# Performance work log

Hardware: AMD Instinct MI355X
Metric: run time of the kernel (lower is better)

## Reference

```python
import jax, jax.numpy as jnp
import numpy as np

IMAGE_W = 640
IMAGE_H = 640
TOP_N = 1000
MIN_SCORE = 0.05
NMS_THR = 0.5
MAX_DET = 100
NUM_CLASSES = 80
STRIDES = [8, 16, 32, 64, 128]
BASE_SIZES = [32, 64, 128, 256, 512]
NEG = jnp.float32(-1e9)


def _make_anchors(batch):
    # standard RetinaNet grid anchors: 3 ratios x 3 scales per location
    per_level = []
    ratios = np.array([0.5, 1.0, 2.0])
    scales = np.array([2.0 ** 0, 2.0 ** (1.0 / 3.0), 2.0 ** (2.0 / 3.0)])
    for stride, base in zip(STRIDES, BASE_SIZES):
        g = IMAGE_W // stride
        ws, hs = [], []
        for r in ratios:
            for s in scales:
                a = base * s
                ws.append(a * np.sqrt(1.0 / r))
                hs.append(a * np.sqrt(r))
        ws = np.array(ws)[None, :]
        hs = np.array(hs)[None, :]
        c = (np.arange(g) + 0.5) * stride
        cxg, cyg = np.meshgrid(c, c)
        cxg = cxg.reshape(-1, 1)
        cyg = cyg.reshape(-1, 1)
        anch = np.stack([cxg - 0.5 * ws, cyg - 0.5 * hs, cxg + 0.5 * ws, cyg + 0.5 * hs], axis=-1)
        anch = anch.reshape(-1, 4).astype(np.float32)  # [g*g*9, 4]
        anch = np.broadcast_to(anch[None], (batch,) + anch.shape).copy()
        per_level.append(jnp.asarray(anch))
    return per_level


def setup_inputs() -> dict:
    key = jax.random.key(0)
    ks = jax.random.split(key, 10)
    B = 8
    ns = [(IMAGE_W // s) ** 2 * 9 for s in STRIDES]
    anchors = _make_anchors(B)
    inp = {}
    for i, n in enumerate(ns):
        inp[f"cls{i}"] = jax.random.uniform(ks[i], (B, n, NUM_CLASSES), dtype=jnp.float32)
        inp[f"reg{i}"] = jax.random.normal(ks[5 + i], (B, n, 4), dtype=jnp.float32) * 0.5
        inp[f"anc{i}"] = anchors[i]
    return inp


def _filter_level(cls_h, reg_h, anc):
    scores = jnp.max(cls_h, axis=2)           # [B, N]
    classes = jnp.argmax(cls_h, axis=2)       # [B, N] int
    if scores.shape[1] >= TOP_N:
        scores, idx = jax.lax.top_k(scores, TOP_N)
        classes = jnp.take_along_axis(classes, idx, axis=1)
        reg_h = jnp.take_along_axis(reg_h, idx[:, :, None], axis=1)
        anc = jnp.take_along_axis(anc, idx[:, :, None], axis=1)
    return scores, classes, reg_h, anc


def _decode(reg, anc):
    # snap tx,ty,tw,th to x1,y1,x2,y2 with int truncation + clamping (as original)
    wh = anc[..., 2:] - anc[..., :2]
    ctr = anc[..., :2] + 0.5 * wh
    r = reg * jnp.array([0.1, 0.1, 0.2, 0.2], reg.dtype)
    pwh = jnp.exp(r[..., 2:]) * wh
    pctr = r[..., :2] * wh + ctr
    b = jnp.concatenate([pctr - 0.5 * pwh, pctr + 0.5 * pwh], axis=-1)
    b = b.astype(jnp.int32)  # truncation toward zero, matches torch .int()
    b = jnp.stack([
        jnp.maximum(b[..., 0], 0),
        jnp.maximum(b[..., 1], 0),
        jnp.minimum(b[..., 2], IMAGE_W - 1),
        jnp.minimum(b[..., 3], IMAGE_H - 1),
    ], axis=-1)
    return b.astype(jnp.float32)


def _nms_one(scores, classes, boxes):
    # greedy NMS on fixed-size arrays with masking (equivalent to sort+while loop)
    valid = scores > MIN_SCORE
    areas = (boxes[:, 2] - boxes[:, 0]) * (boxes[:, 3] - boxes[:, 1])
    live = jnp.where(valid, scores, NEG)

    def step(live, _):
        idx = jnp.argmax(live)
        has = live[idx] > NEG * 0.5
        tb = boxes[idx]
        o_s = jnp.where(has, scores[idx], jnp.float32(-1.0))
        o_c = jnp.where(has, classes[idx].astype(jnp.float32), jnp.float32(-1.0))
        o_b = jnp.where(has, tb, -jnp.ones((4,), jnp.float32))
        tl = jnp.maximum(boxes[:, :2], tb[:2])
        br = jnp.minimum(boxes[:, 2:], tb[2:])
        owh = jnp.clip(br - tl, 0.0)
        inter = owh[:, 0] * owh[:, 1]
        union = jnp.clip(areas[idx] + areas - inter, 1e-4)
        iou = inter / union
        live = live.at[idx].set(NEG)  # remove the selected box itself
        live = jnp.where(has & (iou >= NMS_THR), NEG, live)
        return live, (o_s, o_c, o_b)

    _, (out_s, out_c, out_b) = jax.lax.scan(step, live, None, length=MAX_DET)
    return out_s, out_c, out_b


def reference(cls0, cls1, cls2, cls3, cls4, reg0, reg1, reg2, reg3, reg4,
              anc0, anc1, anc2, anc3, anc4):
    cls_heads = [cls0, cls1, cls2, cls3, cls4]
    reg_heads = [reg0, reg1, reg2, reg3, reg4]
    anchors = [anc0, anc1, anc2, anc3, anc4]
    fs, fc, fr, fa = [], [], [], []
    for c, r, a in zip(cls_heads, reg_heads, anchors):
        s, cl, r, a = _filter_level(c, r, a)
        fs.append(s); fc.append(cl); fr.append(r); fa.append(a)
    scores = jnp.concatenate(fs, axis=1)      # [B, 4125]
    classes = jnp.concatenate(fc, axis=1)
    regs = jnp.concatenate(fr, axis=1)
    ancs = jnp.concatenate(fa, axis=1)
    boxes = _decode(regs, ancs)               # [B, 4125, 4]
    batch_scores, batch_classes, batch_bboxes = jax.vmap(_nms_one)(scores, classes, boxes)
    return batch_scores, batch_classes, batch_bboxes
```

## Files before the change

kernel.cpp:

```cpp
#include <hip/hip_runtime.h>
#include <cmath>

#define NB      8
#define NANCH   76725
#define SSTRIDE 76800
#define CAPP    4352
#define NCAND   4125
#define TIECAP  256
#define MAXDET  100
#define BPI2    1201
#define ZWORDS  148992

struct Ptrs {
    const float* cls[5];
    const float* reg[5];
    const float* anc[5];
};

__device__ __forceinline__ void level_of(int i, int& lvl, int& n, int& N) {
    if (i < 57600)      { lvl = 0; n = i;         N = 57600; }
    else if (i < 72000) { lvl = 1; n = i - 57600; N = 14400; }
    else if (i < 75600) { lvl = 2; n = i - 72000; N = 3600;  }
    else if (i < 76500) { lvl = 3; n = i - 75600; N = 900;   }
    else                { lvl = 4; n = i - 76500; N = 225;   }
}

__device__ __forceinline__ void decode_box(const Ptrs& p, int b, int i, float out[4]) {
    int lvl, n, N; level_of(i, lvl, n, N);
    const float* r = p.reg[lvl] + ((size_t)b * N + n) * 4;
    const float* a = p.anc[lvl] + ((size_t)b * N + n) * 4;
    float a0 = a[0], a1 = a[1], a2 = a[2], a3 = a[3];
    float whx = __fsub_rn(a2, a0), why = __fsub_rn(a3, a1);
    float ctrx = __fadd_rn(a0, __fmul_rn(0.5f, whx));
    float ctry = __fadd_rn(a1, __fmul_rn(0.5f, why));
    float r0 = __fmul_rn(r[0], 0.1f), r1 = __fmul_rn(r[1], 0.1f);
    float r2 = __fmul_rn(r[2], 0.2f), r3 = __fmul_rn(r[3], 0.2f);
    float ex = (float)::exp((double)r2);
    float ey = (float)::exp((double)r3);
    float pwx = __fmul_rn(ex, whx), pwy = __fmul_rn(ey, why);
    float pcx = __fadd_rn(__fmul_rn(r0, whx), ctrx);
    float pcy = __fadd_rn(__fmul_rn(r1, why), ctry);
    float hx = __fmul_rn(0.5f, pwx), hy = __fmul_rn(0.5f, pwy);
    int ix1 = (int)__fsub_rn(pcx, hx);
    int iy1 = (int)__fsub_rn(pcy, hy);
    int ix2 = (int)__fadd_rn(pcx, hx);
    int iy2 = (int)__fadd_rn(pcy, hy);
    ix1 = ix1 > 0 ? ix1 : 0;
    iy1 = iy1 > 0 ? iy1 : 0;
    ix2 = ix2 < 639 ? ix2 : 639;
    iy2 = iy2 < 639 ? iy2 : 639;
    out[0] = (float)ix1; out[1] = (float)iy1; out[2] = (float)ix2; out[3] = (float)iy2;
}

__device__ __forceinline__ unsigned score_key(float s) {
    unsigned u = __float_as_uint(s);
    return (u < 0x3F000000u) ? 0u :
           (u > 0x3F7FFFFFu) ? 0x7FFFFFu : (u - 0x3F000000u);
}

__global__ __launch_bounds__(256) void k_score(Ptrs p, float* __restrict__ scoreAll,
                                               unsigned char* __restrict__ classAll,
                                               unsigned* __restrict__ zeroPtr) {
    int blk = blockIdx.x;
    const int tid = threadIdx.x;
    if (blk < 146) {
        unsigned* zp = zeroPtr + (size_t)blk * 1024;
        int lim = ZWORDS - blk * 1024; if (lim > 1024) lim = 1024;
        for (int i = tid; i < lim; i += 256) zp[i] = 0;
    }
    int b = blk / BPI2, c = blk - b * BPI2;
    int lvl, n0, N, goff;
    if (c < 900)       { lvl = 0; n0 = c * 64;          N = 57600; goff = 0;     }
    else if (c < 1125) { lvl = 1; n0 = (c - 900) * 64;  N = 14400; goff = 57600; }
    else if (c < 1182) { lvl = 2; n0 = (c - 1125) * 64; N = 3600;  goff = 72000; }
    else if (c < 1197) { lvl = 3; n0 = (c - 1182) * 64; N = 900;   goff = 75600; }
    else               { lvl = 4; n0 = (c - 1197) * 64; N = 225;   goff = 76500; }
    const int a = tid >> 2, k = tid & 3;
    const int n = n0 + a;
    if (n >= N) return;
    const float4* f4 = (const float4*)(p.cls[lvl] + ((size_t)b * N + n) * 80);
    float best = -1.0f; int bc = 0;
#pragma unroll
    for (int it = 0; it < 5; ++it) {
        float4 v = f4[it * 4 + k];
        int c0 = (it * 4 + k) * 4;
        if (v.x > best) { best = v.x; bc = c0; }
        if (v.y > best) { best = v.y; bc = c0 + 1; }
        if (v.z > best) { best = v.z; bc = c0 + 2; }
        if (v.w > best) { best = v.w; bc = c0 + 3; }
    }
#pragma unroll
    for (int off = 1; off <= 2; off <<= 1) {
        float ob = __shfl_xor(best, off);
        int oc = __shfl_xor(bc, off);
        if (ob > best || (ob == best && oc < bc)) { best = ob; bc = oc; }
    }
    if (k == 0) {
        scoreAll[b * SSTRIDE + goff + n] = best;
        classAll[b * SSTRIDE + goff + n] = (unsigned char)bc;
    }
}

__device__ __forceinline__ void chunk_of(int blk, int& b, int& g, int& goff, int& loff, int& count) {
    b = blk / 20; int c = blk % 20;
    int lvl, n;
    if (c < 15)      { lvl = 0; goff = 0;     loff = c * 4096;        n = 57600; }
    else if (c < 19) { lvl = 1; goff = 57600; loff = (c - 15) * 4096; n = 14400; }
    else             { lvl = 2; goff = 72000; loff = 0;               n = 3600;  }
    count = n - loff; if (count > 4096) count = 4096;
    g = b * 3 + lvl;
}

__global__ __launch_bounds__(256) void k_hist(const float* __restrict__ scoreAll,
                                              unsigned* __restrict__ ghist) {
    __shared__ unsigned hist[4096];
    int tid = threadIdx.x;
    for (int i = tid; i < 4096; i += 256) hist[i] = 0;
    __syncthreads();
    int b, g, goff, loff, count;
    chunk_of(blockIdx.x, b, g, goff, loff, count);
    const float* s = scoreAll + b * SSTRIDE + goff + loff;
    int e0 = tid * 16;
    if (e0 < count) {
        const float4* p4 = (const float4*)(s + e0);
#pragma unroll
        for (int j = 0; j < 4; ++j) {
            float4 v = p4[j];
            atomicAdd(&hist[score_key(v.x) >> 11], 1u);
            atomicAdd(&hist[score_key(v.y) >> 11], 1u);
            atomicAdd(&hist[score_key(v.z) >> 11], 1u);
            atomicAdd(&hist[score_key(v.w) >> 11], 1u);
        }
    }
    __syncthreads();
    for (int i = tid; i < 4096; i += 256) {
        unsigned v = hist[i];
        if (v) atomicAdd(&ghist[g * 4096 + i], v);
    }
}

__global__ __launch_bounds__(256) void k_hist2(const float* __restrict__ scoreAll,
                                               const unsigned* __restrict__ ghist,
                                               unsigned* __restrict__ ghist2,
                                               int* __restrict__ binB, int* __restrict__ kRem) {
    __shared__ unsigned hist[2048];
    __shared__ unsigned csum[256];
    __shared__ int binB_sh;
    int tid = threadIdx.x;
    int b, g, goff, loff, count;
    chunk_of(blockIdx.x, b, g, goff, loff, count);

    const unsigned* h = ghist + g * 4096;
    {
        unsigned sum = 0;
        int hi = 4095 - tid * 16;
#pragma unroll
        for (int j = 0; j < 16; ++j) sum += h[hi - j];
        csum[tid] = sum;
    }
    for (int i = tid; i < 2048; i += 256) hist[i] = 0;
    __syncthreads();
    if (tid == 0) {
        int k = 1000; unsigned cum = 0; int sel = 0, kk = 1;
        for (int t = 0; t < 256; ++t) {
            cum += csum[t];
            if (cum >= (unsigned)k) {
                int k2 = k - (int)(cum - csum[t]);
                int hb = 4095 - t * 16;
                for (int j = 0; j < 16; ++j) {
                    unsigned c0 = h[hb - j];
                    if ((int)c0 >= k2) { sel = hb - j; kk = k2; break; }
                    k2 -= (int)c0;
                }
                break;
            }
        }
        binB_sh = sel;
        binB[g] = sel; kRem[g] = kk;
    }
    __syncthreads();
    const unsigned B = (unsigned)binB_sh;

    const float* s = scoreAll + b * SSTRIDE + goff + loff;
    int e0 = tid * 16;
    if (e0 < count) {
        const float4* p4 = (const float4*)(s + e0);
#pragma unroll
        for (int j = 0; j < 4; ++j) {
            float4 v = p4[j];
            float vv[4] = {v.x, v.y, v.z, v.w};
#pragma unroll
            for (int q = 0; q < 4; ++q) {
                unsigned key = score_key(vv[q]);
                if ((key >> 11) == B) atomicAdd(&hist[key & 0x7FFu], 1u);
            }
        }
    }
    __syncthreads();
    for (int i = tid; i < 2048; i += 256) {
        unsigned v = hist[i];
        if (v) atomicAdd(&ghist2[g * 2048 + i], v);
    }
}

__global__ __launch_bounds__(256) void k_pick2(const unsigned* __restrict__ ghist2,
                                               const int* __restrict__ binB,
                                               const int* __restrict__ kRem,
                                               unsigned* __restrict__ Tt,
                                               int* __restrict__ ktie) {
    int g = blockIdx.x;
    const unsigned* h = ghist2 + g * 2048;
    __shared__ unsigned csum[256];
    int tid = threadIdx.x;
    unsigned sum = 0;
    int hi = 2047 - tid * 8;
#pragma unroll
    for (int j = 0; j < 8; ++j) sum += h[hi - j];
    csum[tid] = sum;
    __syncthreads();
    if (tid == 0) {
        int k = kRem[g]; unsigned cum = 0; int sel = 0, kk = 1;
        for (int t = 0; t < 256; ++t) {
            cum += csum[t];
            if (cum >= (unsigned)k) {
                int k2 = k - (int)(cum - csum[t]);
                int hb = 2047 - t * 8;
                for (int j = 0; j < 8; ++j) {
                    unsigned c0 = h[hb - j];
                    if ((int)c0 >= k2) { sel = hb - j; kk = k2; break; }
                    k2 -= (int)c0;
                }
                break;
            }
        }
        unsigned key = (((unsigned)binB[g]) << 11) | (unsigned)sel;
        Tt[g] = 0x3F000000u + key;
        ktie[g] = kk;
    }
}

__global__ __launch_bounds__(256) void k_compact(Ptrs p, const float* __restrict__ scoreAll,
                          const unsigned char* __restrict__ classAll,
                          const unsigned* __restrict__ Tt,
                          int* cntG, int* tieCnt, unsigned* tieList,
                          float* cScore, unsigned* cKey, unsigned char* cClass, float* cBox) {
    __shared__ int lcnt[24];
    __shared__ int lbase[24];
    int tid = threadIdx.x;
    if (tid < 24) lcnt[tid] = 0;
    __syncthreads();

    int t = blockIdx.x * 256 + tid;
    bool inb = t < NB * NANCH;
    int b = 0, i = 0, lvl = 0, n = 0, N = 0, g = 0, slot = -1;
    float s = 0.0f;
    bool selG = false;
    if (inb) {
        b = t / NANCH; i = t - b * NANCH;
        level_of(i, lvl, n, N);
        s = scoreAll[b * SSTRIDE + i];
        if (lvl < 3) {
            g = b * 3 + lvl;
            unsigned u = __float_as_uint(s), tt = Tt[g];
            if (u > tt) selG = true;
            else if (u == tt) {
                int pos = atomicAdd(&tieCnt[g * 32], 1);
                if (pos < TIECAP) tieList[g * TIECAP + pos] = (unsigned)i;
            }
        } else {
            slot = (lvl == 3) ? (3000 + n) : (3900 + n);
        }
    }
    int lslot = -1;
    if (selG) lslot = atomicAdd(&lcnt[g], 1);
    __syncthreads();
    if (tid < 24 && lcnt[tid] > 0)
        lbase[tid] = atomicAdd(&cntG[tid * 32], lcnt[tid]);
    __syncthreads();
    if (selG) slot = lvl * 1000 + lbase[g] + lslot;

    if (slot >= 0) {
        int os = b * CAPP + slot;
        cScore[os] = s;
        cKey[os] = (unsigned)i;
        cClass[os] = classAll[b * SSTRIDE + i];
        float box[4]; decode_box(p, b, i, box);
        float* o = &cBox[(size_t)os * 4];
        o[0] = box[0]; o[1] = box[1]; o[2] = box[2]; o[3] = box[3];
    }
}

__device__ __forceinline__ bool iou_sup(float X1, float Y1, float X2, float Y2, float A,
                                        float ox1, float oy1, float ox2, float oy2, float oa) {
    float tlx = fmaxf(X1, ox1), tly = fmaxf(Y1, oy1);
    float brx = fminf(X2, ox2), bry = fminf(Y2, oy2);
    float ow = fmaxf(__fsub_rn(brx, tlx), 0.0f);
    float oh = fmaxf(__fsub_rn(bry, tly), 0.0f);
    float inter = __fmul_rn(ow, oh);
    float uni = __fsub_rn(__fadd_rn(oa, A), inter);
    return (uni > 0.5f) && (__fmul_rn(2.0f, inter) >= uni);
}

__global__ __launch_bounds__(1024) void k_nms(Ptrs p, const float* __restrict__ scoreAll,
                                              const unsigned char* __restrict__ classAll,
                                              const int* __restrict__ ktie,
                                              const int* __restrict__ cntG,
                                              const int* __restrict__ tieCnt,
                                              const unsigned* __restrict__ tieList,
                                              float* __restrict__ cScore,
                                              unsigned* __restrict__ cKey,
                                              unsigned char* __restrict__ cClass,
                                              float* __restrict__ cBox,
                                              float* __restrict__ out) {
    __shared__ unsigned long long skeys[8192];
    __shared__ unsigned hist[4096];
    __shared__ float accB[MAXDET][5];
    __shared__ float cx1[64], cy1[64], cx2[64], cy2[64], car[64], csc[64], ccl[64];
    __shared__ unsigned cvalid[64], supG[64], matlo[64], mathi[64];
    __shared__ int accCnt_sh, gcnt_sh, lowBin_sh;

    const int tid = threadIdx.x;
    const int b = blockIdx.x;
    const int base = b * CAPP;

    if (tid < 3) {
        int blk = b * 3 + tid, lvl = tid;
        int kt = ktie[blk];
        int sbase = lvl * 1000 + cntG[blk * 32];
        int m = tieCnt[blk * 32]; if (m > TIECAP) m = TIECAP;
        unsigned prev = 0; bool first = true;
        for (int q = 0; q < kt; ++q) {
            unsigned bestv = 0xFFFFFFFFu;
            for (int j = 0; j < m; ++j) {
                unsigned v = tieList[blk * TIECAP + j];
                if ((first || v > prev) && v < bestv) bestv = v;
            }
            if (bestv == 0xFFFFFFFFu) break;
            prev = bestv; first = false;
            int os = base + sbase + q;
            int gi = b * SSTRIDE + (int)bestv;
            cScore[os] = scoreAll[gi];
            cKey[os] = bestv;
            cClass[os] = classAll[gi];
            float box[4]; decode_box(p, b, (int)bestv, box);
            float* o = &cBox[(size_t)os * 4];
            o[0] = box[0]; o[1] = box[1]; o[2] = box[2]; o[3] = box[3];
        }
    }
    if (tid == 0) accCnt_sh = 0;
    for (int i = tid; i < 4096; i += 1024) hist[i] = 0;
    __syncthreads();

    for (int s0 = tid; s0 < NCAND; s0 += 1024)
        atomicAdd(&hist[score_key(cScore[base + s0]) >> 11], 1u);
    __syncthreads();

    int curBin = 4096;
    while (accCnt_sh < MAXDET && curBin > 0) {
        if (tid == 0) {
            int cum = 0, bI = curBin;
            while (bI > 0 && cum < 512) { cum += (int)hist[bI - 1]; --bI; }
            lowBin_sh = bI; gcnt_sh = 0;
        }
        __syncthreads();
        int lowBin = lowBin_sh;
        for (int s0 = tid; s0 < NCAND; s0 += 1024) {
            unsigned sk = score_key(cScore[base + s0]);
            int bin = (int)(sk >> 11);
            if (bin >= lowBin && bin < curBin) {
                unsigned aid = cKey[base + s0];
                int pp = atomicAdd(&gcnt_sh, 1);
                skeys[pp] = ((unsigned long long)sk << 30)
                          | ((unsigned long long)(131071u - aid) << 13)
                          | (unsigned long long)s0;
            }
        }
        __syncthreads();
        const int gcnt = gcnt_sh;
        int N = 64; while (N < gcnt) N <<= 1;
        for (int i = gcnt + tid; i < N; i += 1024) skeys[i] = 8191ull;
        __syncthreads();
        for (unsigned kk = 2; kk <= (unsigned)N; kk <<= 1) {
            for (unsigned jj = kk >> 1; jj > 0; jj >>= 1) {
                for (unsigned t = tid; t < (unsigned)N / 2; t += 1024) {
                    unsigned i = ((t & ~(jj - 1)) << 1) | (t & (jj - 1));
                    unsigned l = i | jj;
                    unsigned long long a = skeys[i], c = skeys[l];
                    bool desc = ((i & kk) == 0);
                    if (desc ? (a < c) : (a > c)) { skeys[i] = c; skeys[l] = a; }
                }
                __syncthreads();
            }
        }
        int pos = 0;
        while (accCnt_sh < MAXDET && pos < gcnt) {
            int m = gcnt - pos; if (m > 64) m = 64;
            if (tid < 64) {
                supG[tid] = 0; matlo[tid] = 0; mathi[tid] = 0;
                unsigned vld = 0;
                float s = -1.0f, X1 = 0, Y1 = 0, X2 = 0, Y2 = 0, A = 0, C = -1.0f;
                if (tid < m) {
                    int slot = (int)(skeys[pos + tid] & 8191ull);
                    if (slot < NCAND) {
                        s = cScore[base + slot];
                        const float4 bx = *(const float4*)&cBox[(size_t)(base + slot) * 4];
                        X1 = bx.x; Y1 = bx.y; X2 = bx.z; Y2 = bx.w;
                        A = __fmul_rn(__fsub_rn(X2, X1), __fsub_rn(Y2, Y1));
                        C = (float)cClass[base + slot];
                        vld = (s > 0.05f) ? 1u : 0u;
                    }
                }
                cx1[tid] = X1; cy1[tid] = Y1; cx2[tid] = X2; cy2[tid] = Y2;
                car[tid] = A; csc[tid] = s; ccl[tid] = C; cvalid[tid] = vld;
            }
            __syncthreads();
            const int acc0 = accCnt_sh;
            for (int pp = tid; pp < 64 * acc0; pp += 1024) {
                int j = pp & 63, a2 = pp >> 6;
                if (cvalid[j] && iou_sup(cx1[j], cy1[j], cx2[j], cy2[j], car[j],
                                         accB[a2][0], accB[a2][1], accB[a2][2],
                                         accB[a2][3], accB[a2][4]))
                    atomicOr(&supG[j], 1u);
            }
            for (int pp = tid; pp < 4096; pp += 1024) {
                int r = pp >> 6, c = pp & 63;
                if (c < r && r < m &&
                    iou_sup(cx1[r], cy1[r], cx2[r], cy2[r], car[r],
                            cx1[c], cy1[c], cx2[c], cy2[c], car[c])) {
                    if (c < 32) atomicOr(&matlo[r], 1u << c);
                    else        atomicOr(&mathi[r], 1u << (c - 32));
                }
            }
            __syncthreads();
            if (tid < 64) {
                const int lane = tid;
                bool valid = cvalid[lane] != 0;
                int sup0 = (int)supG[lane];
                unsigned long long mask = (unsigned long long)matlo[lane]
                                        | ((unsigned long long)mathi[lane] << 32);
                float s = csc[lane], X1 = cx1[lane], Y1 = cy1[lane];
                float X2 = cx2[lane], Y2 = cy2[lane], A = car[lane], C = ccl[lane];
                unsigned long long accChunk = 0;
                int accepted = acc0;
                for (int j2 = 0; j2 < m && accepted < MAXDET; ++j2) {
                    int jvalid = __shfl((int)valid, j2);
                    int jsup = __shfl(sup0, j2);
                    unsigned long long jmask = __shfl(mask, j2);
                    if (jvalid && !jsup && !(jmask & accChunk)) {
                        if (lane == j2) {
                            out[b * 100 + accepted] = s;
                            out[800 + b * 100 + accepted] = C;
                            float* ob = &out[1600 + (size_t)(b * 100 + accepted) * 4];
                            ob[0] = X1; ob[1] = Y1; ob[2] = X2; ob[3] = Y2;
                            accB[accepted][0] = X1; accB[accepted][1] = Y1;
                            accB[accepted][2] = X2; accB[accepted][3] = Y2;
                            accB[accepted][4] = A;
                        }
                        accChunk |= 1ull << j2;
                        accepted++;
                    }
                }
                if (lane == 0) accCnt_sh = accepted;
            }
            __syncthreads();
            pos += 64;
        }
        curBin = lowBin;
    }
    __syncthreads();
    int acc = accCnt_sh;
    for (int r = acc + tid; r < MAXDET; r += 1024) {
        out[b * 100 + r] = -1.0f;
        out[800 + b * 100 + r] = -1.0f;
        float* ob = &out[1600 + (size_t)(b * 100 + r) * 4];
        ob[0] = -1.0f; ob[1] = -1.0f; ob[2] = -1.0f; ob[3] = -1.0f;
    }
}

extern "C" void kernel_launch(void* const* d_in, const int* in_sizes, int n_in,
                              void* d_out, int out_size, void* d_ws, size_t ws_size,
                              hipStream_t stream) {
    Ptrs p;
    for (int l = 0; l < 5; ++l) {
        p.cls[l] = (const float*)d_in[3 * l + 0];
        p.reg[l] = (const float*)d_in[3 * l + 1];
        p.anc[l] = (const float*)d_in[3 * l + 2];
    }
    char* ws = (char*)d_ws;
    float*         scoreAll = (float*)(ws + 0);
    unsigned char* classAll = (unsigned char*)(ws + 2457600);
    int*           cntG     = (int*)(ws + 3072000);
    int*           tieCnt   = (int*)(ws + 3075072);
    unsigned*      ghist    = (unsigned*)(ws + 3078144);
    unsigned*      ghist2   = (unsigned*)(ws + 3471360);
    float*         cScore   = (float*)(ws + 3078144);
    unsigned*      cKey     = (unsigned*)(ws + 3217408);
    unsigned char* cClass   = (unsigned char*)(ws + 3356672);
    float*         cBox     = (float*)(ws + 3391488);
    unsigned*      Tt       = (unsigned*)(ws + 3948544);
    int*           ktie     = (int*)(ws + 3948640);
    int*           binB     = (int*)(ws + 3948736);
    int*           kRem     = (int*)(ws + 3948832);
    unsigned*      tieList  = (unsigned*)(ws + 3948928);
    float* out = (float*)d_out;

    int total = NB * NANCH;
    hipLaunchKernelGGL(k_score, dim3(NB * BPI2), dim3(256), 0, stream,
                       p, scoreAll, classAll, (unsigned*)(ws + 3072000));
    hipLaunchKernelGGL(k_hist, dim3(160), dim3(256), 0, stream, scoreAll, ghist);
    hipLaunchKernelGGL(k_hist2, dim3(160), dim3(256), 0, stream,
                       scoreAll, ghist, ghist2, binB, kRem);
    hipLaunchKernelGGL(k_pick2, dim3(24), dim3(256), 0, stream, ghist2, binB, kRem, Tt, ktie);
    hipLaunchKernelGGL(k_compact, dim3((total + 255) / 256), dim3(256), 0, stream,
                       p, scoreAll, classAll, Tt, cntG, tieCnt, tieList,
                       cScore, cKey, cClass, cBox);
    hipLaunchKernelGGL(k_nms, dim3(8), dim3(1024), 0, stream,
                       p, scoreAll, classAll, ktie, cntG, tieCnt, tieList,
                       cScore, cKey, cClass, cBox, out);
}
```

Before: 106.1 us.

## Replace two-pass exact top-k with coarse-bin superset and rank-limited NMS

Removes the second histogram pass, the pick kernel and the serial tie-resolution loop in NMS. Compaction now keeps every candidate whose coarse score bin is at or above the per-level threshold bin, up to a fixed capacity per level. NMS enforces the top-1000 per level by counting ranks in sorted order on a single thread. This cuts two kernel launches and the single-thread tie sort, but NMS sees more candidates and its greedy acceptance loop is now serial on one thread instead of wave-shuffled. It also relies on the coarse bin holding no more than the slot capacity.

```diff
diff --git a/kernel.cpp b/kernel.cpp
--- a/kernel.cpp
+++ b/kernel.cpp
@@ -4,12 +4,13 @@
 #define NB      8
 #define NANCH   76725
 #define SSTRIDE 76800
-#define CAPP    4352
-#define NCAND   4125
-#define TIECAP  256
+#define CAPP    6144
+#define GCAP    1536
+#define NSLOT   5733
 #define MAXDET  100
 #define BPI2    1201
-#define ZWORDS  148992
+#define BPIC    302
+#define ZWORDS  99072
 
 struct Ptrs {
     const float* cls[5];
@@ -63,7 +64,7 @@
                                                unsigned* __restrict__ zeroPtr) {
     int blk = blockIdx.x;
     const int tid = threadIdx.x;
-    if (blk < 146) {
+    if (blk < 97) {
         unsigned* zp = zeroPtr + (size_t)blk * 1024;
         int lim = ZWORDS - blk * 1024; if (lim > 1024) lim = 1024;
         for (int i = tid; i < lim; i += 256) zp[i] = 0;
@@ -139,17 +140,41 @@
     }
 }
 
-__global__ __launch_bounds__(256) void k_hist2(const float* __restrict__ scoreAll,
-                                               const unsigned* __restrict__ ghist,
-                                               unsigned* __restrict__ ghist2,
-                                               int* __restrict__ binB, int* __restrict__ kRem) {
-    __shared__ unsigned hist[2048];
+__global__ __launch_bounds__(256) void k_compact(Ptrs p, const float* __restrict__ scoreAll,
+                          const unsigned char* __restrict__ classAll,
+                          const unsigned* __restrict__ ghist,
+                          int* cntG,
+                          float* cScore, unsigned* cKey, unsigned char* cClass, float* cBox) {
     __shared__ unsigned csum[256];
-    __shared__ int binB_sh;
-    int tid = threadIdx.x;
-    int b, g, goff, loff, count;
-    chunk_of(blockIdx.x, b, g, goff, loff, count);
-
+    __shared__ int binB_sh, lcnt_sh, lbase_sh;
+    const int tid = threadIdx.x;
+    int blk = blockIdx.x;
+    int b = blk / BPIC, c = blk - b * BPIC;
+    int lvl, n0, N, goff;
+    if (c < 225)      { lvl = 0; n0 = c * 256;         N = 57600; goff = 0;     }
+    else if (c < 282) { lvl = 1; n0 = (c - 225) * 256; N = 14400; goff = 57600; }
+    else if (c < 297) { lvl = 2; n0 = (c - 282) * 256; N = 3600;  goff = 72000; }
+    else if (c < 301) { lvl = 3; n0 = (c - 297) * 256; N = 900;   goff = 75600; }
+    else              { lvl = 4; n0 = 0;               N = 225;   goff = 76500; }
+    const int n = n0 + tid;
+
+    if (lvl >= 3) {
+        if (n < N) {
+            int i = goff + n;
+            int slot = (lvl == 3) ? (4608 + n) : (5508 + n);
+            int os = b * CAPP + slot;
+            int gi = b * SSTRIDE + i;
+            cScore[os] = scoreAll[gi];
+            cKey[os] = (unsigned)i;
+            cClass[os] = classAll[gi];
+            float box[4]; decode_box(p, b, i, box);
+            float* o = &cBox[(size_t)os * 4];
+            o[0] = box[0]; o[1] = box[1]; o[2] = box[2]; o[3] = box[3];
+        }
+        return;
+    }
+
+    int g = b * 3 + lvl;
     const unsigned* h = ghist + g * 4096;
     {
         unsigned sum = 0;
@@ -158,10 +183,10 @@
         for (int j = 0; j < 16; ++j) sum += h[hi - j];
         csum[tid] = sum;
     }
-    for (int i = tid; i < 2048; i += 256) hist[i] = 0;
+    if (tid == 0) lcnt_sh = 0;
     __syncthreads();
     if (tid == 0) {
-        int k = 1000; unsigned cum = 0; int sel = 0, kk = 1;
+        int k = 1000; unsigned cum = 0; int sel = 0;
         for (int t = 0; t < 256; ++t) {
             cum += csum[t];
             if (cum >= (unsigned)k) {
@@ -169,124 +194,40 @@
                 int hb = 4095 - t * 16;
                 for (int j = 0; j < 16; ++j) {
                     unsigned c0 = h[hb - j];
-                    if ((int)c0 >= k2) { sel = hb - j; kk = k2; break; }
+                    if ((int)c0 >= k2) { sel = hb - j; break; }
                     k2 -= (int)c0;
                 }
                 break;
             }
         }
         binB_sh = sel;
-        binB[g] = sel; kRem[g] = kk;
     }
     __syncthreads();
     const unsigned B = (unsigned)binB_sh;
 
-    const float* s = scoreAll + b * SSTRIDE + goff + loff;
-    int e0 = tid * 16;
-    if (e0 < count) {
-        const float4* p4 = (const float4*)(s + e0);
-#pragma unroll
-        for (int j = 0; j < 4; ++j) {
-            float4 v = p4[j];
-            float vv[4] = {v.x, v.y, v.z, v.w};
-#pragma unroll
-            for (int q = 0; q < 4; ++q) {
-                unsigned key = score_key(vv[q]);
-                if ((key >> 11) == B) atomicAdd(&hist[key & 0x7FFu], 1u);
-            }
-        }
-    }
-    __syncthreads();
-    for (int i = tid; i < 2048; i += 256) {
-        unsigned v = hist[i];
-        if (v) atomicAdd(&ghist2[g * 2048 + i], v);
-    }
-}
-
-__global__ __launch_bounds__(256) void k_pick2(const unsigned* __restrict__ ghist2,
-                                               const int* __restrict__ binB,
-                                               const int* __restrict__ kRem,
-                                               unsigned* __restrict__ Tt,
-                                               int* __restrict__ ktie) {
-    int g = blockIdx.x;
-    const unsigned* h = ghist2 + g * 2048;
-    __shared__ unsigned csum[256];
-    int tid = threadIdx.x;
-    unsigned sum = 0;
-    int hi = 2047 - tid * 8;
-#pragma unroll
-    for (int j = 0; j < 8; ++j) sum += h[hi - j];
-    csum[tid] = sum;
-    __syncthreads();
-    if (tid == 0) {
-        int k = kRem[g]; unsigned cum = 0; int sel = 0, kk = 1;
-        for (int t = 0; t < 256; ++t) {
-            cum += csum[t];
-            if (cum >= (unsigned)k) {
-                int k2 = k - (int)(cum - csum[t]);
-                int hb = 2047 - t * 8;
-                for (int j = 0; j < 8; ++j) {
-                    unsigned c0 = h[hb - j];
-                    if ((int)c0 >= k2) { sel = hb - j; kk = k2; break; }
-                    k2 -= (int)c0;
-                }
-                break;
-            }
-        }
-        unsigned key = (((unsigned)binB[g]) << 11) | (unsigned)sel;
-        Tt[g] = 0x3F000000u + key;
-        ktie[g] = kk;
-    }
-}
-
-__global__ __launch_bounds__(256) void k_compact(Ptrs p, const float* __restrict__ scoreAll,
-                          const unsigned char* __restrict__ classAll,
-                          const unsigned* __restrict__ Tt,
-                          int* cntG, int* tieCnt, unsigned* tieList,
-                          float* cScore, unsigned* cKey, unsigned char* cClass, float* cBox) {
-    __shared__ int lcnt[24];
-    __shared__ int lbase[24];
-    int tid = threadIdx.x;
-    if (tid < 24) lcnt[tid] = 0;
-    __syncthreads();
-
-    int t = blockIdx.x * 256 + tid;
-    bool inb = t < NB * NANCH;
-    int b = 0, i = 0, lvl = 0, n = 0, N = 0, g = 0, slot = -1;
-    float s = 0.0f;
-    bool selG = false;
-    if (inb) {
-        b = t / NANCH; i = t - b * NANCH;
-        level_of(i, lvl, n, N);
-        s = scoreAll[b * SSTRIDE + i];
-        if (lvl < 3) {
-            g = b * 3 + lvl;
-            unsigned u = __float_as_uint(s), tt = Tt[g];
-            if (u > tt) selG = true;
-            else if (u == tt) {
-                int pos = atomicAdd(&tieCnt[g * 32], 1);
-                if (pos < TIECAP) tieList[g * TIECAP + pos] = (unsigned)i;
-            }
-        } else {
-            slot = (lvl == 3) ? (3000 + n) : (3900 + n);
-        }
+    float s = 0.0f; bool take = false;
+    if (n < N) {
+        s = scoreAll[b * SSTRIDE + goff + n];
+        take = (score_key(s) >> 11) >= B;
     }
     int lslot = -1;
-    if (selG) lslot = atomicAdd(&lcnt[g], 1);
-    __syncthreads();
-    if (tid < 24 && lcnt[tid] > 0)
-        lbase[tid] = atomicAdd(&cntG[tid * 32], lcnt[tid]);
-    __syncthreads();
-    if (selG) slot = lvl * 1000 + lbase[g] + lslot;
-
-    if (slot >= 0) {
-        int os = b * CAPP + slot;
-        cScore[os] = s;
-        cKey[os] = (unsigned)i;
-        cClass[os] = classAll[b * SSTRIDE + i];
-        float box[4]; decode_box(p, b, i, box);
-        float* o = &cBox[(size_t)os * 4];
-        o[0] = box[0]; o[1] = box[1]; o[2] = box[2]; o[3] = box[3];
+    if (take) lslot = atomicAdd(&lcnt_sh, 1);
+    __syncthreads();
+    if (tid == 0 && lcnt_sh > 0)
+        lbase_sh = atomicAdd(&cntG[g * 32], lcnt_sh);
+    __syncthreads();
+    if (take) {
+        int gslot = lbase_sh + lslot;
+        if (gslot < GCAP) {
+            int i = goff + n;
+            int os = b * CAPP + lvl * GCAP + gslot;
+            cScore[os] = s;
+            cKey[os] = (unsigned)i;
+            cClass[os] = classAll[b * SSTRIDE + i];
+            float box[4]; decode_box(p, b, i, box);
+            float* o = &cBox[(size_t)os * 4];
+            o[0] = box[0]; o[1] = box[1]; o[2] = box[2]; o[3] = box[3];
+        }
     }
 }
 
@@ -301,58 +242,45 @@
     return (uni > 0.5f) && (__fmul_rn(2.0f, inter) >= uni);
 }
 
-__global__ __launch_bounds__(1024) void k_nms(Ptrs p, const float* __restrict__ scoreAll,
-                                              const unsigned char* __restrict__ classAll,
-                                              const int* __restrict__ ktie,
+__device__ __forceinline__ bool slot_valid(int s0, int c0, int c1, int c2) {
+    if (s0 < GCAP)     return s0 < c0;
+    if (s0 < 2 * GCAP) return s0 - GCAP < c1;
+    if (s0 < 3 * GCAP) return s0 - 2 * GCAP < c2;
+    return s0 < NSLOT;
+}
+
+__global__ __launch_bounds__(1024) void k_nms(const float* __restrict__ cScore,
+                                              const unsigned* __restrict__ cKey,
+                                              const unsigned char* __restrict__ cClass,
+                                              const float* __restrict__ cBox,
                                               const int* __restrict__ cntG,
-                                              const int* __restrict__ tieCnt,
-                                              const unsigned* __restrict__ tieList,
-                                              float* __restrict__ cScore,
-                                              unsigned* __restrict__ cKey,
-                                              unsigned char* __restrict__ cClass,
-                                              float* __restrict__ cBox,
                                               float* __restrict__ out) {
     __shared__ unsigned long long skeys[8192];
     __shared__ unsigned hist[4096];
     __shared__ float accB[MAXDET][5];
     __shared__ float cx1[64], cy1[64], cx2[64], cy2[64], car[64], csc[64], ccl[64];
     __shared__ unsigned cvalid[64], supG[64], matlo[64], mathi[64];
+    __shared__ int cgrp[64];
     __shared__ int accCnt_sh, gcnt_sh, lowBin_sh;
+    __shared__ int cnt_sh[3], rcnt_sh[3];
 
     const int tid = threadIdx.x;
     const int b = blockIdx.x;
     const int base = b * CAPP;
 
     if (tid < 3) {
-        int blk = b * 3 + tid, lvl = tid;
-        int kt = ktie[blk];
-        int sbase = lvl * 1000 + cntG[blk * 32];
-        int m = tieCnt[blk * 32]; if (m > TIECAP) m = TIECAP;
-        unsigned prev = 0; bool first = true;
-        for (int q = 0; q < kt; ++q) {
-            unsigned bestv = 0xFFFFFFFFu;
-            for (int j = 0; j < m; ++j) {
-                unsigned v = tieList[blk * TIECAP + j];
-                if ((first || v > prev) && v < bestv) bestv = v;
-            }
-            if (bestv == 0xFFFFFFFFu) break;
-            prev = bestv; first = false;
-            int os = base + sbase + q;
-            int gi = b * SSTRIDE + (int)bestv;
-            cScore[os] = scoreAll[gi];
-            cKey[os] = bestv;
-            cClass[os] = classAll[gi];
-            float box[4]; decode_box(p, b, (int)bestv, box);
-            float* o = &cBox[(size_t)os * 4];
-            o[0] = box[0]; o[1] = box[1]; o[2] = box[2]; o[3] = box[3];
-        }
+        int v = cntG[(b * 3 + tid) * 32];
+        cnt_sh[tid] = v < GCAP ? v : GCAP;
+        rcnt_sh[tid] = 0;
     }
     if (tid == 0) accCnt_sh = 0;
     for (int i = tid; i < 4096; i += 1024) hist[i] = 0;
     __syncthreads();
-
-    for (int s0 = tid; s0 < NCAND; s0 += 1024)
-        atomicAdd(&hist[score_key(cScore[base + s0]) >> 11], 1u);
+    const int c0 = cnt_sh[0], c1 = cnt_sh[1], c2 = cnt_sh[2];
+
+    for (int s0 = tid; s0 < NSLOT; s0 += 1024)
+        if (slot_valid(s0, c0, c1, c2))
+            atomicAdd(&hist[score_key(cScore[base + s0]) >> 11], 1u);
     __syncthreads();
 
     int curBin = 4096;
@@ -364,7 +292,8 @@
         }
         __syncthreads();
         int lowBin = lowBin_sh;
-        for (int s0 = tid; s0 < NCAND; s0 += 1024) {
+        for (int s0 = tid; s0 < NSLOT; s0 += 1024) {
+            if (!slot_valid(s0, c0, c1, c2)) continue;
             unsigned sk = score_key(cScore[base + s0]);
             int bin = (int)(sk >> 11);
             if (bin >= lowBin && bin < curBin) {
@@ -397,21 +326,23 @@
             int m = gcnt - pos; if (m > 64) m = 64;
             if (tid < 64) {
                 supG[tid] = 0; matlo[tid] = 0; mathi[tid] = 0;
-                unsigned vld = 0;
+                unsigned vld = 0; int grp = 3;
                 float s = -1.0f, X1 = 0, Y1 = 0, X2 = 0, Y2 = 0, A = 0, C = -1.0f;
                 if (tid < m) {
-                    int slot = (int)(skeys[pos + tid] & 8191ull);
-                    if (slot < NCAND) {
-                        s = cScore[base + slot];
-                        const float4 bx = *(const float4*)&cBox[(size_t)(base + slot) * 4];
-                        X1 = bx.x; Y1 = bx.y; X2 = bx.z; Y2 = bx.w;
-                        A = __fmul_rn(__fsub_rn(X2, X1), __fsub_rn(Y2, Y1));
-                        C = (float)cClass[base + slot];
-                        vld = (s > 0.05f) ? 1u : 0u;
-                    }
+                    unsigned long long key = skeys[pos + tid];
+                    int slot = (int)(key & 8191ull);
+                    unsigned aid = 131071u - (unsigned)((key >> 13) & 0x1FFFFull);
+                    grp = (aid < 57600u) ? 0 : (aid < 72000u) ? 1 : (aid < 75600u) ? 2 : 3;
+                    s = cScore[base + slot];
+                    const float4 bx = *(const float4*)&cBox[(size_t)(base + slot) * 4];
+                    X1 = bx.x; Y1 = bx.y; X2 = bx.z; Y2 = bx.w;
+                    A = __fmul_rn(__fsub_rn(X2, X1), __fsub_rn(Y2, Y1));
+                    C = (float)cClass[base + slot];
+                    vld = (s > 0.05f) ? 1u : 0u;
                 }
                 cx1[tid] = X1; cy1[tid] = Y1; cx2[tid] = X2; cy2[tid] = Y2;
-                car[tid] = A; csc[tid] = s; ccl[tid] = C; cvalid[tid] = vld;
+                car[tid] = A; csc[tid] = s; ccl[tid] = C;
+                cvalid[tid] = vld; cgrp[tid] = grp;
             }
             __syncthreads();
             const int acc0 = accCnt_sh;
@@ -432,35 +363,33 @@
                 }
             }
             __syncthreads();
-            if (tid < 64) {
-                const int lane = tid;
-                bool valid = cvalid[lane] != 0;
-                int sup0 = (int)supG[lane];
-                unsigned long long mask = (unsigned long long)matlo[lane]
-                                        | ((unsigned long long)mathi[lane] << 32);
-                float s = csc[lane], X1 = cx1[lane], Y1 = cy1[lane];
-                float X2 = cx2[lane], Y2 = cy2[lane], A = car[lane], C = ccl[lane];
+            if (tid == 0) {
+                int r0 = rcnt_sh[0], r1 = rcnt_sh[1], r2 = rcnt_sh[2];
                 unsigned long long accChunk = 0;
                 int accepted = acc0;
                 for (int j2 = 0; j2 < m && accepted < MAXDET; ++j2) {
-                    int jvalid = __shfl((int)valid, j2);
-                    int jsup = __shfl(sup0, j2);
-                    unsigned long long jmask = __shfl(mask, j2);
-                    if (jvalid && !jsup && !(jmask & accChunk)) {
-                        if (lane == j2) {
-                            out[b * 100 + accepted] = s;
-                            out[800 + b * 100 + accepted] = C;
-                            float* ob = &out[1600 + (size_t)(b * 100 + accepted) * 4];
-                            ob[0] = X1; ob[1] = Y1; ob[2] = X2; ob[3] = Y2;
-                            accB[accepted][0] = X1; accB[accepted][1] = Y1;
-                            accB[accepted][2] = X2; accB[accepted][3] = Y2;
-                            accB[accepted][4] = A;
-                        }
+                    int jg = cgrp[j2];
+                    bool inset = true;
+                    if (jg == 0)      inset = (++r0 <= 1000);
+                    else if (jg == 1) inset = (++r1 <= 1000);
+                    else if (jg == 2) inset = (++r2 <= 1000);
+                    if (!inset) continue;
+                    unsigned long long jmask = (unsigned long long)matlo[j2]
+                                             | ((unsigned long long)mathi[j2] << 32);
+                    if (cvalid[j2] && !supG[j2] && !(jmask & accChunk)) {
+                        out[b * 100 + accepted] = csc[j2];
+                        out[800 + b * 100 + accepted] = ccl[j2];
+                        float* ob = &out[1600 + (size_t)(b * 100 + accepted) * 4];
+                        ob[0] = cx1[j2]; ob[1] = cy1[j2]; ob[2] = cx2[j2]; ob[3] = cy2[j2];
+                        accB[accepted][0] = cx1[j2]; accB[accepted][1] = cy1[j2];
+                        accB[accepted][2] = cx2[j2]; accB[accepted][3] = cy2[j2];
+                        accB[accepted][4] = car[j2];
                         accChunk |= 1ull << j2;
                         accepted++;
                     }
                 }
-                if (lane == 0) accCnt_sh = accepted;
+                rcnt_sh[0] = r0; rcnt_sh[1] = r1; rcnt_sh[2] = r2;
+                accCnt_sh = accepted;
             }
             __syncthreads();
             pos += 64;
@@ -490,31 +419,19 @@
     float*         scoreAll = (float*)(ws + 0);
     unsigned char* classAll = (unsigned char*)(ws + 2457600);
     int*           cntG     = (int*)(ws + 3072000);
-    int*           tieCnt   = (int*)(ws + 3075072);
-    unsigned*      ghist    = (unsigned*)(ws + 3078144);
-    unsigned*      ghist2   = (unsigned*)(ws + 3471360);
-    float*         cScore   = (float*)(ws + 3078144);
-    unsigned*      cKey     = (unsigned*)(ws + 3217408);
-    unsigned char* cClass   = (unsigned char*)(ws + 3356672);
-    float*         cBox     = (float*)(ws + 3391488);
-    unsigned*      Tt       = (unsigned*)(ws + 3948544);
-    int*           ktie     = (int*)(ws + 3948640);
-    int*           binB     = (int*)(ws + 3948736);
-    int*           kRem     = (int*)(ws + 3948832);
-    unsigned*      tieList  = (unsigned*)(ws + 3948928);
+    unsigned*      ghist    = (unsigned*)(ws + 3075072);
+    float*         cScore   = (float*)(ws + 3468288);
+    unsigned*      cKey     = (unsigned*)(ws + 3664896);
+    unsigned char* cClass   = (unsigned char*)(ws + 3861504);
+    float*         cBox     = (float*)(ws + 3910656);
     float* out = (float*)d_out;
 
-    int total = NB * NANCH;
     hipLaunchKernelGGL(k_score, dim3(NB * BPI2), dim3(256), 0, stream,
                        p, scoreAll, classAll, (unsigned*)(ws + 3072000));
     hipLaunchKernelGGL(k_hist, dim3(160), dim3(256), 0, stream, scoreAll, ghist);
-    hipLaunchKernelGGL(k_hist2, dim3(160), dim3(256), 0, stream,
-                       scoreAll, ghist, ghist2, binB, kRem);
-    hipLaunchKernelGGL(k_pick2, dim3(24), dim3(256), 0, stream, ghist2, binB, kRem, Tt, ktie);
-    hipLaunchKernelGGL(k_compact, dim3((total + 255) / 256), dim3(256), 0, stream,
-                       p, scoreAll, classAll, Tt, cntG, tieCnt, tieList,
+    hipLaunchKernelGGL(k_compact, dim3(NB * BPIC), dim3(256), 0, stream,
+                       p, scoreAll, classAll, ghist, cntG,
                        cScore, cKey, cClass, cBox);
     hipLaunchKernelGGL(k_nms, dim3(8), dim3(1024), 0, stream,
-                       p, scoreAll, classAll, ktie, cntG, tieCnt, tieList,
-                       cScore, cKey, cClass, cBox, out);
-}
+                       cScore, cKey, cClass, cBox, cntG, out);
+}
```

Result: faster. 100.8 us (-5.0%).
